# Kernel tuning notes

Measured on AMD Instinct MI355X. Metric: run time of the kernel, lower is better.

## Reference

```python
import jax, jax.numpy as jnp
import numpy as np

NP_, NA_, NS_ = 200000, 30000, 50000
D = 128          # embed_dim == hidden_dim
P = 128          # projection_dim
L = 3            # num GNN layers
R = 6            # num relations
LN_EPS = 1e-5
L2_EPS = 1e-12

# relation order matches metadata[1]: (src_type, dst_type, n_src, n_dst, n_edges)
RELS = [
    ("artist", "performance", NA_, NP_, 400000),      # performs
    ("performance", "song", NP_, NS_, 400000),        # performing
    ("artist", "song", NA_, NS_, 150000),             # composed
    ("performance", "artist", NP_, NA_, 400000),      # rev_performs
    ("song", "performance", NS_, NP_, 400000),        # rev_performing
    ("song", "artist", NS_, NA_, 150000),             # rev_composed
]
NNODES = {"performance": NP_, "artist": NA_, "song": NS_}


def _segment_mean(src, idx, n):
    # src: [E, D] messages, idx: [E] destination ids
    s = jax.ops.segment_sum(src, idx, num_segments=n)
    c = jax.ops.segment_sum(jnp.ones((src.shape[0], 1), src.dtype), idx, num_segments=n)
    return s / jnp.maximum(c, 1.0)


def _l2norm(x):
    n = jnp.linalg.norm(x, axis=-1, keepdims=True)
    return x / jnp.maximum(n, L2_EPS)


def _layernorm(x, g, b):
    mu = jnp.mean(x, axis=-1, keepdims=True)
    var = jnp.mean(jnp.square(x - mu), axis=-1, keepdims=True)
    return (x - mu) * jax.lax.rsqrt(var + LN_EPS) * g + b


def setup_inputs() -> dict:
    key = jax.random.key(0)
    ks = list(jax.random.split(key, 32))
    ki = iter(ks)
    inp = {}
    inp["perf_nid"] = jnp.arange(NP_, dtype=jnp.int32)
    inp["artist_nid"] = jnp.arange(NA_, dtype=jnp.int32)
    inp["song_nid"] = jnp.arange(NS_, dtype=jnp.int32)
    enames = ["e_performs", "e_performing", "e_composed",
              "e_rev_performs", "e_rev_performing", "e_rev_composed"]
    for name, (s, t, n_src, n_dst, n_e) in zip(enames, RELS):
        src = jax.random.randint(next(ki), (n_e,), 0, n_src, dtype=jnp.int32)
        dst = jax.random.randint(next(ki), (n_e,), 0, n_dst, dtype=jnp.int32)
        inp[name] = jnp.stack([src, dst])  # [2, E]
    inp["emb_performance"] = jax.random.normal(next(ki), (NP_, D), jnp.float32)
    inp["emb_artist"] = jax.random.normal(next(ki), (NA_, D), jnp.float32)
    inp["emb_song"] = jax.random.normal(next(ki), (NS_, D), jnp.float32)
    sc = 1.0 / np.sqrt(D)
    inp["Wl"] = jax.random.normal(next(ki), (L, R, D, D), jnp.float32) * sc
    inp["bl"] = jnp.zeros((L, R, D), jnp.float32)
    inp["Wr"] = jax.random.normal(next(ki), (L, R, D, D), jnp.float32) * sc
    inp["ln_g"] = jnp.ones((3, D), jnp.float32)
    inp["ln_b"] = jnp.zeros((3, D), jnp.float32)
    inp["pw1"] = jax.random.normal(next(ki), (3, D, P), jnp.float32) * sc
    inp["pb1"] = jnp.zeros((3, P), jnp.float32)
    inp["pw2"] = jax.random.normal(next(ki), (3, P, P), jnp.float32) * (1.0 / np.sqrt(P))
    inp["pb2"] = jnp.zeros((3, P), jnp.float32)
    return inp


def _forward(perf_nid, artist_nid, song_nid, edges,
             emb_performance, emb_artist, emb_song,
             Wl, bl, Wr, ln_g, ln_b, pw1, pb1, pw2, pb2):
    x = {
        "performance": emb_performance[perf_nid],
        "artist": emb_artist[artist_nid],
        "song": emb_song[song_nid],
    }
    for layer in range(L):
        new = {t: 0.0 for t in x}
        for r, ((s, t, _, _, _), e) in enumerate(zip(RELS, edges)):
            # SAGEConv: lin_l(mean_agg(x_src)) + lin_r(x_dst), then L2 normalize
            msg = _segment_mean(x[s][e[0]], e[1], x[t].shape[0])
            out = msg @ Wl[layer, r] + bl[layer, r] + x[t] @ Wr[layer, r]
            new[t] = new[t] + _l2norm(out)  # HeteroConv aggr='sum'
        x = new
        if layer < L - 1:
            x = {t: jax.nn.relu(v) for t, v in x.items()}
    res = []
    for i, t in enumerate(["performance", "artist", "song"]):
        h = _layernorm(x[t], ln_g[i], ln_b[i])
        h = jax.nn.relu(h @ pw1[i] + pb1[i]) @ pw2[i] + pb2[i]
        res.append(_l2norm(h))
    return tuple(res)


def reference(perf_nid, artist_nid, song_nid,
              e_performs, e_performing, e_composed,
              e_rev_performs, e_rev_performing, e_rev_composed,
              emb_performance, emb_artist, emb_song,
              Wl, bl, Wr, ln_g, ln_b, pw1, pb1, pw2, pb2):
    edges = [e_performs, e_performing, e_composed,
             e_rev_performs, e_rev_performing, e_rev_composed]
    return _forward(perf_nid, artist_nid, song_nid, edges,
                    emb_performance, emb_artist, emb_song,
                    Wl, bl, Wr, ln_g, ln_b, pw1, pb1, pw2, pb2)
```

## Files before the change

kernel.cpp:

```cpp
#include <hip/hip_runtime.h>
#include <math.h>


#define NPF 200000
#define NAR 30000
#define NSO 50000
#define NDTOT 560000
#define ETOT  1900000
#define VPT 12
#define SCAN_CHUNK (256 * VPT)
#define SCAN_NB 183

#define BLKP 3125
#define BLKA 469
#define BLKS 782
#define BLKTOT (BLKP + BLKA + BLKS)

typedef __attribute__((ext_vector_type(8))) short bf16x8;
typedef __attribute__((ext_vector_type(4))) float f32x4;

__device__ __forceinline__ unsigned short f2bf(float f) {
  union { float f; unsigned u; } v; v.f = f;
  unsigned u = v.u;
  u += 0x7FFFu + ((u >> 16) & 1u);
  return (unsigned short)(u >> 16);
}
__device__ __forceinline__ float bf2f(unsigned short h) {
  union { unsigned u; float f; } v; v.u = ((unsigned)h) << 16;
  return v.f;
}

struct BF3 { short h, m, l; };
__device__ __forceinline__ BF3 split3(float f) {
  BF3 r;
  unsigned short hh = f2bf(f);
  float r1 = f - bf2f(hh);
  unsigned short mm = f2bf(r1);
  float r2 = r1 - bf2f(mm);
  r.h = (short)hh; r.m = (short)mm; r.l = (short)f2bf(r2);
  return r;
}

#define MFMA6(ah, am, al, bh, bm, blo, acc)                                     \
  acc = __builtin_amdgcn_mfma_f32_16x16x32_bf16(ah, bh, acc, 0, 0, 0);          \
  acc = __builtin_amdgcn_mfma_f32_16x16x32_bf16(am, bh, acc, 0, 0, 0);          \
  acc = __builtin_amdgcn_mfma_f32_16x16x32_bf16(ah, bm, acc, 0, 0, 0);          \
  acc = __builtin_amdgcn_mfma_f32_16x16x32_bf16(al, bh, acc, 0, 0, 0);          \
  acc = __builtin_amdgcn_mfma_f32_16x16x32_bf16(am, bm, acc, 0, 0, 0);          \
  acc = __builtin_amdgcn_mfma_f32_16x16x32_bf16(ah, blo, acc, 0, 0, 0);

__device__ __forceinline__ void blk_decode(int b, int* t, int* lb) {
  if (b < BLKP)             { *t = 0; *lb = b; }
  else if (b < BLKP + BLKA) { *t = 1; *lb = b - BLKP; }
  else                      { *t = 2; *lb = b - BLKP - BLKA; }
}

__global__ void k_gather_all(const int* __restrict__ nidP, const int* __restrict__ nidA,
                             const int* __restrict__ nidS,
                             const float4* __restrict__ embP, const float4* __restrict__ embA,
                             const float4* __restrict__ embS, float4* __restrict__ dst) {
  int i = blockIdx.x * blockDim.x + threadIdx.x;
  if (i >= 280000 * 32) return;
  int r = i >> 5, c = i & 31;
  const int* nid; const float4* emb; int lr;
  if (r < NPF)            { nid = nidP; emb = embP; lr = r; }
  else if (r < NPF + NAR) { nid = nidA; emb = embA; lr = r - NPF; }
  else                    { nid = nidS; emb = embS; lr = r - NPF - NAR; }
  dst[(size_t)r * 32 + c] = emb[(size_t)nid[lr] * 32 + c];
}

__device__ __forceinline__ void edge_decode(int i,
    const int* e0, const int* e1, const int* e2, const int* e3, const int* e4, const int* e5,
    const int** eg, int* lo, int* E, int* co) {
  if (i < 400000)       { *eg = e0; *lo = i;           *E = 400000; *co = 0; }
  else if (i < 800000)  { *eg = e1; *lo = i - 400000;  *E = 400000; *co = 200000; }
  else if (i < 950000)  { *eg = e2; *lo = i - 800000;  *E = 150000; *co = 250000; }
  else if (i < 1350000) { *eg = e3; *lo = i - 950000;  *E = 400000; *co = 300000; }
  else if (i < 1750000) { *eg = e4; *lo = i - 1350000; *E = 400000; *co = 330000; }
  else                  { *eg = e5; *lo = i - 1750000; *E = 150000; *co = 530000; }
}

__global__ void k_count_all(const int* e0, const int* e1, const int* e2,
                            const int* e3, const int* e4, const int* e5,
                            int* __restrict__ cnt) {
  int i = blockIdx.x * blockDim.x + threadIdx.x;
  if (i >= ETOT) return;
  const int* eg; int lo, E, co;
  edge_decode(i, e0, e1, e2, e3, e4, e5, &eg, &lo, &E, &co);
  atomicAdd(&cnt[co + eg[E + lo]], 1);
}

__global__ void k_scan_block(const int* __restrict__ cnt, int n, int* __restrict__ part) {
  __shared__ int sd[256];
  int t = threadIdx.x;
  int base = blockIdx.x * SCAN_CHUNK + t * VPT;
  int s = 0;
#pragma unroll
  for (int i = 0; i < VPT; ++i) { int idx = base + i; if (idx < n) s += cnt[idx]; }
  sd[t] = s; __syncthreads();
  for (int off = 128; off > 0; off >>= 1) { if (t < off) sd[t] += sd[t + off]; __syncthreads(); }
  if (t == 0) part[blockIdx.x] = sd[0];
}

__global__ void k_scan_top(int* part, int nb) {
  __shared__ int sd[256];
  int t = threadIdx.x;
  int v = (t < nb) ? part[t] : 0;
  sd[t] = v; __syncthreads();
  for (int off = 1; off < 256; off <<= 1) {
    int add = (t >= off) ? sd[t - off] : 0;
    __syncthreads();
    sd[t] += add;
    __syncthreads();
  }
  if (t < nb) part[t] = sd[t] - v;
}

__global__ void k_scan_final(int* __restrict__ cnt, int n, const int* __restrict__ part,
                             int* __restrict__ rp, int E) {
  __shared__ int sd[256];
  int t = threadIdx.x;
  int base = blockIdx.x * SCAN_CHUNK + t * VPT;
  int v[VPT]; int s = 0;
#pragma unroll
  for (int i = 0; i < VPT; ++i) { int idx = base + i; v[i] = (idx < n) ? cnt[idx] : 0; s += v[i]; }
  sd[t] = s; __syncthreads();
  for (int off = 1; off < 256; off <<= 1) {
    int add = (t >= off) ? sd[t - off] : 0;
    __syncthreads();
    sd[t] += add;
    __syncthreads();
  }
  int run = part[blockIdx.x] + sd[t] - s;
#pragma unroll
  for (int i = 0; i < VPT; ++i) {
    int idx = base + i;
    if (idx < n) { rp[idx] = run; cnt[idx] = 0; }
    run += v[i];
  }
  if (blockIdx.x == 0 && t == 0) rp[n] = E;
}

__global__ void k_fill_all(const int* e0, const int* e1, const int* e2,
                           const int* e3, const int* e4, const int* e5,
                           const int* __restrict__ rp, int* __restrict__ cur,
                           int* __restrict__ col) {
  int i = blockIdx.x * blockDim.x + threadIdx.x;
  if (i >= ETOT) return;
  const int* eg; int lo, E, co;
  edge_decode(i, e0, e1, e2, e3, e4, e5, &eg, &lo, &E, &co);
  int d = co + eg[E + lo];
  int p = atomicAdd(&cur[d], 1);
  col[rp[d] + p] = eg[lo];
}

#define PKSTRIDE 49152
__global__ void k_packW(const float* __restrict__ Wl, const float* __restrict__ Wr,
                        const float* __restrict__ pw1, const float* __restrict__ pw2,
                        unsigned short* __restrict__ pk) {
  int gid = blockIdx.x * blockDim.x + threadIdx.x;
  if (gid >= 42 * 4 * 8 * 64) return;
  int lane = gid & 63;
  int t = (gid >> 6) & 7;
  int s = (gid >> 9) & 3;
  int m = gid >> 11;
  const float* src;
  if (m < 18) src = Wl + (size_t)m * 16384;
  else if (m < 36) src = Wr + (size_t)(m - 18) * 16384;
  else if (m < 39) src = pw1 + (size_t)(m - 36) * 16384;
  else src = pw2 + (size_t)(m - 39) * 16384;
  int n = t * 16 + (lane & 15);
  int k0 = s * 32 + (lane >> 4) * 8;
  unsigned short* hi = pk + (size_t)m * PKSTRIDE + ((size_t)(s * 8 + t) * 64 + lane) * 8;
  unsigned short* mid = hi + 16384;
  unsigned short* lo = hi + 32768;
#pragma unroll
  for (int j = 0; j < 8; ++j) {
    float f = src[(size_t)(k0 + j) * 128 + n];
    BF3 w = split3(f);
    hi[j] = (unsigned short)w.h;
    mid[j] = (unsigned short)w.m;
    lo[j] = (unsigned short)w.l;
  }
}

__global__ __launch_bounds__(256) void k_sage_merged(
    const int* __restrict__ rp, const int* __restrict__ col,
    const float* __restrict__ xin, float* __restrict__ xout,
    const unsigned short* __restrict__ pkw, const float* __restrict__ bl,
    int layer, int slot, int relu_out) {
  __shared__ float Ms[64 * 128];
  static const int RELSLOT[2][3] = {{0, 3, 1}, {4, 5, 2}};
  static const int SRCT[2][3]    = {{1, 0, 0}, {2, 2, 1}};
  static const int CNT_OFF[6] = {0, 200000, 250000, 300000, 330000, 530000};
  static const int TOFFc[3] = {0, NPF, NPF + NAR};
  static const int TNc[3]   = {NPF, NAR, NSO};
  int ty, lb;
  blk_decode(blockIdx.x, &ty, &lb);
  int rel = RELSLOT[slot][ty];
  int m = layer * 6 + rel;
  const int* rpt = rp + CNT_OFF[rel];
  const float* xsrc = xin + (size_t)TOFFc[SRCT[slot][ty]] * 128;
  const float* xdst = xin + (size_t)TOFFc[ty] * 128;
  float* outp = xout + (size_t)TOFFc[ty] * 128;
  const unsigned short* pkl = pkw + (size_t)m * PKSTRIDE;
  const unsigned short* pkr = pkw + (size_t)(18 + m) * PKSTRIDE;
  const float* blv = bl + (size_t)m * 128;
  int n_dst = TNc[ty];
  int first = (slot == 0);

  int lane = threadIdx.x & 63;
  int wave = threadIdx.x >> 6;
  int row0b = lb * 64;

  {
    int g = lane >> 4, li = lane & 15;
    int c0 = li * 8;
    int bb[4], ne[4];
    int maxd = 0;
#pragma unroll
    for (int i = 0; i < 4; ++i) {
      int d = row0b + wave * 16 + g * 4 + i;
      int b = 0, e = 0;
      if (d < n_dst) { b = rpt[d]; e = rpt[d + 1]; }
      bb[i] = b; ne[i] = e - b;
      maxd = max(maxd, e - b);
    }
    f32x4 a0[4], a1[4];
#pragma unroll
    for (int i = 0; i < 4; ++i) { a0[i] = (f32x4){0.f,0.f,0.f,0.f}; a1[i] = (f32x4){0.f,0.f,0.f,0.f}; }
    int nc[4];
#pragma unroll
    for (int i = 0; i < 4; ++i) nc[i] = (0 < ne[i]) ? col[bb[i]] : 0;
    for (int k = 0; k < maxd; ++k) {
      int cc[4];
#pragma unroll
      for (int i = 0; i < 4; ++i) cc[i] = nc[i];
#pragma unroll
      for (int i = 0; i < 4; ++i) nc[i] = (k + 1 < ne[i]) ? col[bb[i] + k + 1] : 0;
#pragma unroll
      for (int i = 0; i < 4; ++i) {
        if (k < ne[i]) {
          const float* sp = xsrc + (size_t)cc[i] * 128 + c0;
          float4 v0 = *(const float4*)sp;
          float4 v1 = *(const float4*)(sp + 4);
          a0[i][0] += v0.x; a0[i][1] += v0.y; a0[i][2] += v0.z; a0[i][3] += v0.w;
          a1[i][0] += v1.x; a1[i][1] += v1.y; a1[i][2] += v1.z; a1[i][3] += v1.w;
        }
      }
    }
#pragma unroll
    for (int i = 0; i < 4; ++i) {
      float inv = (ne[i] > 0) ? 1.0f / (float)ne[i] : 0.0f;
      int lr = wave * 16 + g * 4 + i;
      float4* Mrow = (float4*)&Ms[lr * 128];
      int sw = lr & 7;
      Mrow[(li * 2) ^ sw]     = make_float4(a0[i][0]*inv, a0[i][1]*inv, a0[i][2]*inv, a0[i][3]*inv);
      Mrow[(li * 2 + 1) ^ sw] = make_float4(a1[i][0]*inv, a1[i][1]*inv, a1[i][2]*inv, a1[i][3]*inv);
    }
  }

  int row0 = row0b + wave * 16;
  int cg = lane & 15, qg = lane >> 4;
  int ar = min(row0 + cg, n_dst - 1);
  int lar = wave * 16 + cg;
  int kb = qg * 8;
  const float4* Mlar = (const float4*)&Ms[lar * 128];
  int swl = lar & 7;

  f32x4 acc[8];
#pragma unroll
  for (int t = 0; t < 8; ++t) acc[t] = (f32x4){0.f, 0.f, 0.f, 0.f};

#pragma unroll
  for (int sm = 0; sm < 2; ++sm) {
    const unsigned short* pk = sm ? pkr : pkl;
#pragma unroll
    for (int s = 0; s < 4; ++s) {
      float4 f0, f1;
      if (sm) {
        const float* ap = xdst + (size_t)ar * 128 + s * 32 + kb;
        f0 = *(const float4*)ap;
        f1 = *(const float4*)(ap + 4);
      } else {
        int ch = s * 8 + qg * 2;
        f0 = Mlar[ch ^ swl];
        f1 = Mlar[(ch + 1) ^ swl];
      }
      float fa[8] = {f0.x, f0.y, f0.z, f0.w, f1.x, f1.y, f1.z, f1.w};
      bf16x8 ah, am, al;
#pragma unroll
      for (int j = 0; j < 8; ++j) {
        BF3 w = split3(fa[j]);
        ah[j] = w.h; am[j] = w.m; al[j] = w.l;
      }
      const unsigned short* pb = pk + (size_t)s * 4096 + (size_t)lane * 8;
#pragma unroll
      for (int t = 0; t < 8; ++t) {
        bf16x8 bh  = *(const bf16x8*)(pb + (size_t)t * 512);
        bf16x8 bm  = *(const bf16x8*)(pb + (size_t)t * 512 + 16384);
        bf16x8 blo = *(const bf16x8*)(pb + (size_t)t * 512 + 32768);
        MFMA6(ah, am, al, bh, bm, blo, acc[t]);
      }
    }
  }

#pragma unroll
  for (int t = 0; t < 8; ++t) {
    float bv = blv[t * 16 + cg];
#pragma unroll
    for (int j = 0; j < 4; ++j) acc[t][j] += bv;
  }
  float ss[4];
#pragma unroll
  for (int j = 0; j < 4; ++j) {
    float s = 0.f;
#pragma unroll
    for (int t = 0; t < 8; ++t) s += acc[t][j] * acc[t][j];
    s += __shfl_xor(s, 1); s += __shfl_xor(s, 2);
    s += __shfl_xor(s, 4); s += __shfl_xor(s, 8);
    ss[j] = 1.0f / fmaxf(sqrtf(s), 1e-12f);
  }
#pragma unroll
  for (int j = 0; j < 4; ++j) {
    int r = row0 + qg * 4 + j;
    if (r < n_dst) {
      float* p = outp + (size_t)r * 128 + cg;
      if (first) {
#pragma unroll
        for (int t = 0; t < 8; ++t) p[t * 16] = acc[t][j] * ss[j];
      } else {
#pragma unroll
        for (int t = 0; t < 8; ++t) {
          float v = p[t * 16] + acc[t][j] * ss[j];
          if (relu_out) v = fmaxf(v, 0.f);
          p[t * 16] = v;
        }
      }
    }
  }
}

__global__ __launch_bounds__(256) void k_ln_all(const float* __restrict__ in,
                                                float* __restrict__ out,
                                                const float* __restrict__ lng,
                                                const float* __restrict__ lnb) {
  int gid = blockIdx.x * blockDim.x + threadIdx.x;
  int r = gid >> 2, q = gid & 3;
  if (r >= NPF + NAR + NSO) return;
  int ty = (r < NPF) ? 0 : ((r < NPF + NAR) ? 1 : 2);
  const float* g = lng + ty * 128;
  const float* bvec = lnb + ty * 128;
  float v[32];
#pragma unroll
  for (int j = 0; j < 8; ++j) {
    float4 t4 = *(const float4*)(in + (size_t)r * 128 + q * 32 + j * 4);
    v[4 * j] = t4.x; v[4 * j + 1] = t4.y; v[4 * j + 2] = t4.z; v[4 * j + 3] = t4.w;
  }
  float s = 0.f, sq = 0.f;
#pragma unroll
  for (int j = 0; j < 32; ++j) { s += v[j]; sq += v[j] * v[j]; }
  s  += __shfl_xor(s, 1);  s  += __shfl_xor(s, 2);
  sq += __shfl_xor(sq, 1); sq += __shfl_xor(sq, 2);
  float mu = s * 0.0078125f;
  float var = sq * 0.0078125f - mu * mu;
  float rs = rsqrtf(var + 1e-5f);
#pragma unroll
  for (int j = 0; j < 8; ++j) {
    float o[4];
#pragma unroll
    for (int k = 0; k < 4; ++k) {
      int c = q * 32 + j * 4 + k;
      o[k] = (v[j * 4 + k] - mu) * rs * g[c] + bvec[c];
    }
    *(float4*)(out + (size_t)r * 128 + q * 32 + j * 4) = make_float4(o[0], o[1], o[2], o[3]);
  }
}

__global__ __launch_bounds__(256) void k_gemm_all(
    const float* __restrict__ A, const unsigned short* __restrict__ pkw,
    const float* __restrict__ biasb, float* __restrict__ outp,
    int pkbase, int relu, int l2n) {
  static const int TOFFc[3] = {0, NPF, NPF + NAR};
  static const int TNc[3]   = {NPF, NAR, NSO};
  int ty, lb;
  blk_decode(blockIdx.x, &ty, &lb);
  const unsigned short* pk = pkw + (size_t)(pkbase + ty) * PKSTRIDE;
  const float* bias = biasb + ty * 128;
  const float* At = A + (size_t)TOFFc[ty] * 128;
  float* outt = outp + (size_t)TOFFc[ty] * 128;
  int n = TNc[ty];

  int lane = threadIdx.x & 63;
  int wave = threadIdx.x >> 6;
  int row0 = lb * 64 + wave * 16;
  int cg = lane & 15, qg = lane >> 4;
  int ar = min(row0 + cg, n - 1);
  int kb = qg * 8;

  f32x4 acc[8];
#pragma unroll
  for (int t = 0; t < 8; ++t) acc[t] = (f32x4){0.f, 0.f, 0.f, 0.f};

#pragma unroll
  for (int s = 0; s < 4; ++s) {
    const float* ap = At + (size_t)ar * 128 + s * 32 + kb;
    float4 f0 = *(const float4*)ap;
    float4 f1 = *(const float4*)(ap + 4);
    float fa[8] = {f0.x, f0.y, f0.z, f0.w, f1.x, f1.y, f1.z, f1.w};
    bf16x8 ah, am, al;
#pragma unroll
    for (int j = 0; j < 8; ++j) {
      BF3 w = split3(fa[j]);
      ah[j] = w.h; am[j] = w.m; al[j] = w.l;
    }
    const unsigned short* pb = pk + (size_t)s * 4096 + (size_t)lane * 8;
#pragma unroll
    for (int t = 0; t < 8; ++t) {
      bf16x8 bh  = *(const bf16x8*)(pb + (size_t)t * 512);
      bf16x8 bm  = *(const bf16x8*)(pb + (size_t)t * 512 + 16384);
      bf16x8 blo = *(const bf16x8*)(pb + (size_t)t * 512 + 32768);
      MFMA6(ah, am, al, bh, bm, blo, acc[t]);
    }
  }

#pragma unroll
  for (int t = 0; t < 8; ++t) {
    float bv = bias[t * 16 + cg];
#pragma unroll
    for (int j = 0; j < 4; ++j) acc[t][j] += bv;
  }

  float ss[4];
  if (l2n) {
#pragma unroll
    for (int j = 0; j < 4; ++j) {
      float s = 0.f;
#pragma unroll
      for (int t = 0; t < 8; ++t) s += acc[t][j] * acc[t][j];
      s += __shfl_xor(s, 1); s += __shfl_xor(s, 2);
      s += __shfl_xor(s, 4); s += __shfl_xor(s, 8);
      ss[j] = 1.0f / fmaxf(sqrtf(s), 1e-12f);
    }
  } else {
#pragma unroll
    for (int j = 0; j < 4; ++j) ss[j] = 1.0f;
  }

#pragma unroll
  for (int j = 0; j < 4; ++j) {
    int r = row0 + qg * 4 + j;
    if (r < n) {
      float* p = outt + (size_t)r * 128 + cg;
#pragma unroll
      for (int t = 0; t < 8; ++t) {
        float v = acc[t][j] * ss[j];
        if (relu) v = fmaxf(v, 0.f);
        p[t * 16] = v;
      }
    }
  }
}

extern "C" void kernel_launch(void* const* d_in, const int* in_sizes, int n_in,
                              void* d_out, int out_size, void* d_ws, size_t ws_size,
                              hipStream_t stream) {
  const int* nid[3] = {(const int*)d_in[0], (const int*)d_in[1], (const int*)d_in[2]};
  const int* eg[6];
  for (int r = 0; r < 6; ++r) eg[r] = (const int*)d_in[3 + r];
  const float* emb[3] = {(const float*)d_in[9], (const float*)d_in[10], (const float*)d_in[11]};
  const float* Wl  = (const float*)d_in[12];
  const float* bl  = (const float*)d_in[13];
  const float* Wr  = (const float*)d_in[14];
  const float* lng = (const float*)d_in[15];
  const float* lnb = (const float*)d_in[16];
  const float* pw1 = (const float*)d_in[17];
  const float* pb1 = (const float*)d_in[18];
  const float* pw2 = (const float*)d_in[19];
  const float* pb2 = (const float*)d_in[20];

  float* cur = (float*)d_ws;
  int* col   = (int*)(cur + (size_t)280000 * 128);
  int* rp    = col + ETOT;
  int* cnt   = rp + NDTOT + 1;
  int* part  = cnt + NDTOT;
  size_t pk_off = ((size_t)((char*)(part + 256) - (char*)d_ws) + 255) & ~(size_t)255;
  unsigned short* pkw = (unsigned short*)((char*)d_ws + pk_off);
  float* dout = (float*)d_out;

  k_packW<<<dim3(336), dim3(256), 0, stream>>>(Wl, Wr, pw1, pw2, pkw);

  k_gather_all<<<dim3((280000 * 32 + 255) / 256), dim3(256), 0, stream>>>(
      nid[0], nid[1], nid[2],
      (const float4*)emb[0], (const float4*)emb[1], (const float4*)emb[2],
      (float4*)cur);

  hipMemsetAsync(cnt, 0, (size_t)NDTOT * 4, stream);
  k_count_all<<<dim3((ETOT + 255) / 256), dim3(256), 0, stream>>>(
      eg[0], eg[1], eg[2], eg[3], eg[4], eg[5], cnt);
  k_scan_block<<<dim3(SCAN_NB), dim3(256), 0, stream>>>(cnt, NDTOT, part);
  k_scan_top<<<dim3(1), dim3(256), 0, stream>>>(part, SCAN_NB);
  k_scan_final<<<dim3(SCAN_NB), dim3(256), 0, stream>>>(cnt, NDTOT, part, rp, ETOT);
  k_fill_all<<<dim3((ETOT + 255) / 256), dim3(256), 0, stream>>>(
      eg[0], eg[1], eg[2], eg[3], eg[4], eg[5], rp, cnt, col);

  for (int layer = 0; layer < 3; ++layer) {
    float* xin  = (layer == 1) ? dout : cur;
    float* xout = (layer == 1) ? cur  : dout;
    int relu_o = (layer < 2) ? 1 : 0;
    k_sage_merged<<<dim3(BLKTOT), dim3(256), 0, stream>>>(
        rp, col, xin, xout, pkw, bl, layer, 0, relu_o);
    k_sage_merged<<<dim3(BLKTOT), dim3(256), 0, stream>>>(
        rp, col, xin, xout, pkw, bl, layer, 1, relu_o);
  }

  k_ln_all<<<dim3((280000 * 4 + 255) / 256), dim3(256), 0, stream>>>(
      dout, cur, lng, lnb);
  k_gemm_all<<<dim3(BLKTOT), dim3(256), 0, stream>>>(
      cur, pkw, pb1, cur, 36, 1, 0);
  k_gemm_all<<<dim3(BLKTOT), dim3(256), 0, stream>>>(
      cur, pkw, pb2, dout, 39, 0, 1);

  (void)in_sizes; (void)n_in; (void)out_size; (void)ws_size;
}
```

Baseline: 2.093 ms.

## Split fused SAGE aggregation+GEMM into separate aggregate and GEMM kernels

Replaces the merged kernel, which did neighbor mean-aggregation into shared memory and then the bf16x3 MFMA GEMM, with two kernels. The first aggregates into a global message buffer and the second reads it for the GEMM. Launches are split per node-type group so the message buffer stays small, and it reuses the count/scan workspace. The aim is to stop the gather phase and the GEMM phase from limiting each other's occupancy (the old kernel used 32KB of LDS). The cost is an extra global write and read of the messages and four times as many launches.

```diff
diff --git a/kernel.cpp b/kernel.cpp
--- a/kernel.cpp
+++ b/kernel.cpp
@@ -15,6 +15,7 @@
 #define BLKA 469
 #define BLKS 782
 #define BLKTOT (BLKP + BLKA + BLKS)
+#define BLKG1 (BLKA + BLKS)
 
 typedef __attribute__((ext_vector_type(8))) short bf16x8;
 typedef __attribute__((ext_vector_type(4))) float f32x4;
@@ -48,12 +49,6 @@
   acc = __builtin_amdgcn_mfma_f32_16x16x32_bf16(al, bh, acc, 0, 0, 0);          \
   acc = __builtin_amdgcn_mfma_f32_16x16x32_bf16(am, bm, acc, 0, 0, 0);          \
   acc = __builtin_amdgcn_mfma_f32_16x16x32_bf16(ah, blo, acc, 0, 0, 0);
-
-__device__ __forceinline__ void blk_decode(int b, int* t, int* lb) {
-  if (b < BLKP)             { *t = 0; *lb = b; }
-  else if (b < BLKP + BLKA) { *t = 1; *lb = b - BLKP; }
-  else                      { *t = 2; *lb = b - BLKP - BLKA; }
-}
 
 __global__ void k_gather_all(const int* __restrict__ nidP, const int* __restrict__ nidA,
                              const int* __restrict__ nidS,
@@ -184,89 +179,105 @@
   }
 }
 
-__global__ __launch_bounds__(256) void k_sage_merged(
+__device__ __forceinline__ void grp_decode(int b, int grp, int* ty, int* lb,
+                                           int* msgbase, int* n_dst) {
+  if (grp == 0)      { *ty = 0; *lb = b; *msgbase = 0; *n_dst = NPF; }
+  else if (b < BLKA) { *ty = 1; *lb = b; *msgbase = 0; *n_dst = NAR; }
+  else               { *ty = 2; *lb = b - BLKA; *msgbase = NAR; *n_dst = NSO; }
+}
+
+__global__ __launch_bounds__(256) void k_agg1(
     const int* __restrict__ rp, const int* __restrict__ col,
-    const float* __restrict__ xin, float* __restrict__ xout,
-    const unsigned short* __restrict__ pkw, const float* __restrict__ bl,
-    int layer, int slot, int relu_out) {
-  __shared__ float Ms[64 * 128];
+    const float* __restrict__ xin, float* __restrict__ msg,
+    int slot, int grp) {
   static const int RELSLOT[2][3] = {{0, 3, 1}, {4, 5, 2}};
   static const int SRCT[2][3]    = {{1, 0, 0}, {2, 2, 1}};
   static const int CNT_OFF[6] = {0, 200000, 250000, 300000, 330000, 530000};
   static const int TOFFc[3] = {0, NPF, NPF + NAR};
-  static const int TNc[3]   = {NPF, NAR, NSO};
-  int ty, lb;
-  blk_decode(blockIdx.x, &ty, &lb);
+  int ty, lb, msgbase, n_dst;
+  grp_decode(blockIdx.x, grp, &ty, &lb, &msgbase, &n_dst);
+  int rel = RELSLOT[slot][ty];
+  const int* rpt = rp + CNT_OFF[rel];
+  const float* xsrc = xin + (size_t)TOFFc[SRCT[slot][ty]] * 128;
+
+  int lane = threadIdx.x & 63;
+  int wave = threadIdx.x >> 6;
+  int row0b = lb * 64;
+  int g = lane >> 4, li = lane & 15;
+  int c0 = li * 8;
+
+  int bb[4], ne[4], dd[4];
+  int maxd = 0;
+#pragma unroll
+  for (int i = 0; i < 4; ++i) {
+    int d = row0b + wave * 16 + g * 4 + i;
+    dd[i] = d;
+    int b = 0, e = 0;
+    if (d < n_dst) { b = rpt[d]; e = rpt[d + 1]; }
+    bb[i] = b; ne[i] = e - b;
+    maxd = max(maxd, e - b);
+  }
+  f32x4 a0[4], a1[4];
+#pragma unroll
+  for (int i = 0; i < 4; ++i) { a0[i] = (f32x4){0.f,0.f,0.f,0.f}; a1[i] = (f32x4){0.f,0.f,0.f,0.f}; }
+  int nc[4];
+#pragma unroll
+  for (int i = 0; i < 4; ++i) nc[i] = (0 < ne[i]) ? col[bb[i]] : 0;
+  for (int k = 0; k < maxd; ++k) {
+    int cc[4];
+#pragma unroll
+    for (int i = 0; i < 4; ++i) cc[i] = nc[i];
+#pragma unroll
+    for (int i = 0; i < 4; ++i) nc[i] = (k + 1 < ne[i]) ? col[bb[i] + k + 1] : 0;
+#pragma unroll
+    for (int i = 0; i < 4; ++i) {
+      if (k < ne[i]) {
+        const float* sp = xsrc + (size_t)cc[i] * 128 + c0;
+        float4 v0 = *(const float4*)sp;
+        float4 v1 = *(const float4*)(sp + 4);
+        a0[i][0] += v0.x; a0[i][1] += v0.y; a0[i][2] += v0.z; a0[i][3] += v0.w;
+        a1[i][0] += v1.x; a1[i][1] += v1.y; a1[i][2] += v1.z; a1[i][3] += v1.w;
+      }
+    }
+  }
+#pragma unroll
+  for (int i = 0; i < 4; ++i) {
+    if (dd[i] < n_dst) {
+      float inv = (ne[i] > 0) ? 1.0f / (float)ne[i] : 0.0f;
+      float* mp = msg + (size_t)(msgbase + dd[i]) * 128 + c0;
+      *(float4*)mp       = make_float4(a0[i][0]*inv, a0[i][1]*inv, a0[i][2]*inv, a0[i][3]*inv);
+      *(float4*)(mp + 4) = make_float4(a1[i][0]*inv, a1[i][1]*inv, a1[i][2]*inv, a1[i][3]*inv);
+    }
+  }
+}
+
+__global__ __launch_bounds__(256) void k_sage_gemm(
+    const float* __restrict__ msg, const float* __restrict__ xin,
+    float* __restrict__ xout, const unsigned short* __restrict__ pkw,
+    const float* __restrict__ bl, int layer, int slot, int grp, int relu_out) {
+  static const int RELSLOT[2][3] = {{0, 3, 1}, {4, 5, 2}};
+  static const int CNT_OFF[6] = {0, 200000, 250000, 300000, 330000, 530000};
+  static const int TOFFc[3] = {0, NPF, NPF + NAR};
+  (void)CNT_OFF;
+  int ty, lb, msgbase, n_dst;
+  grp_decode(blockIdx.x, grp, &ty, &lb, &msgbase, &n_dst);
   int rel = RELSLOT[slot][ty];
   int m = layer * 6 + rel;
-  const int* rpt = rp + CNT_OFF[rel];
-  const float* xsrc = xin + (size_t)TOFFc[SRCT[slot][ty]] * 128;
-  const float* xdst = xin + (size_t)TOFFc[ty] * 128;
-  float* outp = xout + (size_t)TOFFc[ty] * 128;
   const unsigned short* pkl = pkw + (size_t)m * PKSTRIDE;
   const unsigned short* pkr = pkw + (size_t)(18 + m) * PKSTRIDE;
   const float* blv = bl + (size_t)m * 128;
-  int n_dst = TNc[ty];
+  const float* xdst = xin + (size_t)TOFFc[ty] * 128;
+  float* outp = xout + (size_t)TOFFc[ty] * 128;
   int first = (slot == 0);
 
   int lane = threadIdx.x & 63;
   int wave = threadIdx.x >> 6;
-  int row0b = lb * 64;
-
-  {
-    int g = lane >> 4, li = lane & 15;
-    int c0 = li * 8;
-    int bb[4], ne[4];
-    int maxd = 0;
-#pragma unroll
-    for (int i = 0; i < 4; ++i) {
-      int d = row0b + wave * 16 + g * 4 + i;
-      int b = 0, e = 0;
-      if (d < n_dst) { b = rpt[d]; e = rpt[d + 1]; }
-      bb[i] = b; ne[i] = e - b;
-      maxd = max(maxd, e - b);
-    }
-    f32x4 a0[4], a1[4];
-#pragma unroll
-    for (int i = 0; i < 4; ++i) { a0[i] = (f32x4){0.f,0.f,0.f,0.f}; a1[i] = (f32x4){0.f,0.f,0.f,0.f}; }
-    int nc[4];
-#pragma unroll
-    for (int i = 0; i < 4; ++i) nc[i] = (0 < ne[i]) ? col[bb[i]] : 0;
-    for (int k = 0; k < maxd; ++k) {
-      int cc[4];
-#pragma unroll
-      for (int i = 0; i < 4; ++i) cc[i] = nc[i];
-#pragma unroll
-      for (int i = 0; i < 4; ++i) nc[i] = (k + 1 < ne[i]) ? col[bb[i] + k + 1] : 0;
-#pragma unroll
-      for (int i = 0; i < 4; ++i) {
-        if (k < ne[i]) {
-          const float* sp = xsrc + (size_t)cc[i] * 128 + c0;
-          float4 v0 = *(const float4*)sp;
-          float4 v1 = *(const float4*)(sp + 4);
-          a0[i][0] += v0.x; a0[i][1] += v0.y; a0[i][2] += v0.z; a0[i][3] += v0.w;
-          a1[i][0] += v1.x; a1[i][1] += v1.y; a1[i][2] += v1.z; a1[i][3] += v1.w;
-        }
-      }
-    }
-#pragma unroll
-    for (int i = 0; i < 4; ++i) {
-      float inv = (ne[i] > 0) ? 1.0f / (float)ne[i] : 0.0f;
-      int lr = wave * 16 + g * 4 + i;
-      float4* Mrow = (float4*)&Ms[lr * 128];
-      int sw = lr & 7;
-      Mrow[(li * 2) ^ sw]     = make_float4(a0[i][0]*inv, a0[i][1]*inv, a0[i][2]*inv, a0[i][3]*inv);
-      Mrow[(li * 2 + 1) ^ sw] = make_float4(a1[i][0]*inv, a1[i][1]*inv, a1[i][2]*inv, a1[i][3]*inv);
-    }
-  }
-
-  int row0 = row0b + wave * 16;
+  int row0 = lb * 64 + wave * 16;
   int cg = lane & 15, qg = lane >> 4;
   int ar = min(row0 + cg, n_dst - 1);
-  int lar = wave * 16 + cg;
   int kb = qg * 8;
-  const float4* Mlar = (const float4*)&Ms[lar * 128];
-  int swl = lar & 7;
+  const float* msgrow = msg + (size_t)(msgbase + ar) * 128;
+  const float* xrow   = xdst + (size_t)ar * 128;
 
   f32x4 acc[8];
 #pragma unroll
@@ -275,18 +286,12 @@
 #pragma unroll
   for (int sm = 0; sm < 2; ++sm) {
     const unsigned short* pk = sm ? pkr : pkl;
+    const float* arow = sm ? xrow : msgrow;
 #pragma unroll
     for (int s = 0; s < 4; ++s) {
-      float4 f0, f1;
-      if (sm) {
-        const float* ap = xdst + (size_t)ar * 128 + s * 32 + kb;
-        f0 = *(const float4*)ap;
-        f1 = *(const float4*)(ap + 4);
-      } else {
-        int ch = s * 8 + qg * 2;
-        f0 = Mlar[ch ^ swl];
-        f1 = Mlar[(ch + 1) ^ swl];
-      }
+      const float* ap = arow + s * 32 + kb;
+      float4 f0 = *(const float4*)ap;
+      float4 f1 = *(const float4*)(ap + 4);
       float fa[8] = {f0.x, f0.y, f0.z, f0.w, f1.x, f1.y, f1.z, f1.w};
       bf16x8 ah, am, al;
 #pragma unroll
@@ -384,7 +389,9 @@
   static const int TOFFc[3] = {0, NPF, NPF + NAR};
   static const int TNc[3]   = {NPF, NAR, NSO};
   int ty, lb;
-  blk_decode(blockIdx.x, &ty, &lb);
+  if (blockIdx.x < BLKP)             { ty = 0; lb = blockIdx.x; }
+  else if (blockIdx.x < BLKP + BLKA) { ty = 1; lb = blockIdx.x - BLKP; }
+  else                               { ty = 2; lb = blockIdx.x - BLKP - BLKA; }
   const unsigned short* pk = pkw + (size_t)(pkbase + ty) * PKSTRIDE;
   const float* bias = biasb + ty * 128;
   const float* At = A + (size_t)TOFFc[ty] * 128;
@@ -482,10 +489,12 @@
   float* cur = (float*)d_ws;
   int* col   = (int*)(cur + (size_t)280000 * 128);
   int* rp    = col + ETOT;
-  int* cnt   = rp + NDTOT + 1;
+  size_t pk_off = ((size_t)((char*)(rp + NDTOT + 1) - (char*)d_ws) + 255) & ~(size_t)255;
+  unsigned short* pkw = (unsigned short*)((char*)d_ws + pk_off);
+  size_t sc_off = ((size_t)((char*)(pkw + 42 * PKSTRIDE) - (char*)d_ws) + 255) & ~(size_t)255;
+  float* msg = (float*)((char*)d_ws + sc_off);
+  int* cnt   = (int*)msg;
   int* part  = cnt + NDTOT;
-  size_t pk_off = ((size_t)((char*)(part + 256) - (char*)d_ws) + 255) & ~(size_t)255;
-  unsigned short* pkw = (unsigned short*)((char*)d_ws + pk_off);
   float* dout = (float*)d_out;
 
   k_packW<<<dim3(336), dim3(256), 0, stream>>>(Wl, Wr, pw1, pw2, pkw);
@@ -508,10 +517,14 @@
     float* xin  = (layer == 1) ? dout : cur;
     float* xout = (layer == 1) ? cur  : dout;
     int relu_o = (layer < 2) ? 1 : 0;
-    k_sage_merged<<<dim3(BLKTOT), dim3(256), 0, stream>>>(
-        rp, col, xin, xout, pkw, bl, layer, 0, relu_o);
-    k_sage_merged<<<dim3(BLKTOT), dim3(256), 0, stream>>>(
-        rp, col, xin, xout, pkw, bl, layer, 1, relu_o);
+    for (int slot = 0; slot < 2; ++slot) {
+      k_agg1<<<dim3(BLKP), dim3(256), 0, stream>>>(rp, col, xin, msg, slot, 0);
+      k_sage_gemm<<<dim3(BLKP), dim3(256), 0, stream>>>(
+          msg, xin, xout, pkw, bl, layer, slot, 0, relu_o);
+      k_agg1<<<dim3(BLKG1), dim3(256), 0, stream>>>(rp, col, xin, msg, slot, 1);
+      k_sage_gemm<<<dim3(BLKG1), dim3(256), 0, stream>>>(
+          msg, xin, xout, pkw, bl, layer, slot, 1, relu_o);
+    }
   }
 
   k_ln_all<<<dim3((280000 * 4 + 255) / 256), dim3(256), 0, stream>>>(
```

Result: slower. 2.602 ms (+24.3%).
